# Kernel tuning notes

Measured on AMD Instinct MI355X. Metric: run time of the kernel, lower is better.

The kernel has to match this reference:

```python
import jax, jax.numpy as jnp
import numpy as np

N_HEAD = 16
N_KV_HEAD = 4
N_EMBD = 2048
HEAD_DIM = N_EMBD // N_HEAD  # 128
RMS_EPS = float(np.finfo(np.float32).eps)  # torch F.rms_norm default eps


def _apply_rotary(x, cos, sin):
    # x: [B,T,H,D]; cos/sin: [1,T,1,D/2]
    d = x.shape[-1] // 2
    x1, x2 = x[..., :d], x[..., d:]
    y1 = x1 * cos + x2 * sin
    y2 = -x1 * sin + x2 * cos
    return jnp.concatenate([y1, y2], axis=-1)


def _rms_norm(x):
    var = jnp.mean(jnp.square(x), axis=-1, keepdims=True)
    return x * jax.lax.rsqrt(var + RMS_EPS)


def setup_inputs() -> dict:
    key = jax.random.key(0)
    ks = jax.random.split(key, 7)
    B, T = 2, 2048
    x = jax.random.normal(ks[0], (B, T, N_EMBD), dtype=jnp.float32)
    cos = jax.random.normal(ks[1], (1, T, 1, HEAD_DIM // 2), dtype=jnp.float32)
    sin = jax.random.normal(ks[2], (1, T, 1, HEAD_DIM // 2), dtype=jnp.float32)
    s = 1.0 / np.sqrt(N_EMBD)
    Wq = jax.random.normal(ks[3], (N_HEAD * HEAD_DIM, N_EMBD), dtype=jnp.float32) * s
    Wk = jax.random.normal(ks[4], (N_KV_HEAD * HEAD_DIM, N_EMBD), dtype=jnp.float32) * s
    Wv = jax.random.normal(ks[5], (N_KV_HEAD * HEAD_DIM, N_EMBD), dtype=jnp.float32) * s
    Wo = jax.random.normal(ks[6], (N_EMBD, N_EMBD), dtype=jnp.float32) * s
    return {"x": x, "cos": cos, "sin": sin, "Wq": Wq, "Wk": Wk, "Wv": Wv, "Wo": Wo}


def reference(x, cos, sin, Wq, Wk, Wv, Wo):
    B, T, C = x.shape
    q = (x @ Wq.T).reshape(B, T, N_HEAD, HEAD_DIM)
    k = (x @ Wk.T).reshape(B, T, N_KV_HEAD, HEAD_DIM)
    v = (x @ Wv.T).reshape(B, T, N_KV_HEAD, HEAD_DIM)
    q = _rms_norm(_apply_rotary(q, cos, sin))
    k = _rms_norm(_apply_rotary(k, cos, sin))
    # to [B,H,T,D]; expand kv heads for GQA
    q = q.transpose(0, 2, 1, 3)
    k = k.transpose(0, 2, 1, 3)
    v = v.transpose(0, 2, 1, 3)
    g = N_HEAD // N_KV_HEAD
    k = jnp.repeat(k, g, axis=1)
    v = jnp.repeat(v, g, axis=1)
    scale = 1.0 / np.sqrt(HEAD_DIM)
    scores = jnp.einsum("bhtd,bhsd->bhts", q, k) * scale
    causal = jnp.tril(jnp.ones((T, T), dtype=bool))
    scores = jnp.where(causal, scores, -jnp.inf)
    attn = jax.nn.softmax(scores, axis=-1)
    y = jnp.einsum("bhts,bhsd->bhtd", attn, v)
    y = y.transpose(0, 2, 1, 3).reshape(B, T, C)
    return y @ Wo.T
```

## Files before the change

kernel.cpp:

```cpp
#include <hip/hip_runtime.h>
#include <hip/hip_bf16.h>
#include <stdint.h>

#define B_   2
#define T_   2048
#define CEMB 2048
#define H_   16
#define HKV_ 4
#define D_   128

typedef __attribute__((ext_vector_type(8))) short bf16x8;
typedef __attribute__((ext_vector_type(4))) float f32x4;
typedef __attribute__((ext_vector_type(16))) float f32x16;

#if __has_builtin(__builtin_amdgcn_exp2f)
#define EXP2(x) __builtin_amdgcn_exp2f(x)
#else
#define EXP2(x) exp2f(x)
#endif

__device__ __forceinline__ unsigned short f2b(float f) {
  union { float f; unsigned u; } v; v.f = f;
  unsigned r = v.u + 0x7FFFu + ((v.u >> 16) & 1u);
  return (unsigned short)(r >> 16);
}
__device__ __forceinline__ float b2f(unsigned short u) {
  union { unsigned u; float f; } v; v.u = ((unsigned)u) << 16; return v.f;
}
__device__ __forceinline__ unsigned cvtpk(float lo, float hi) {
  unsigned r;
  asm("v_cvt_pk_bf16_f32 %0, %1, %2" : "=v"(r) : "v"(lo), "v"(hi));
  return r;
}

#if __has_builtin(__builtin_amdgcn_permlane32_swap)
__device__ __forceinline__ void pl32(unsigned& a, unsigned& b) {
  auto r = __builtin_amdgcn_permlane32_swap(a, b, false, false);
  a = r[0]; b = r[1];
}
#else
__device__ __forceinline__ void pl32(unsigned& a, unsigned& b) {
  const bool hih = (threadIdx.x & 32) != 0;
  unsigned sa = __shfl_xor(a, 32), sb = __shfl_xor(b, 32);
  unsigned na = hih ? sb : a;
  unsigned nb = hih ? b : sa;
  a = na; b = nb;
}
#endif

__device__ __forceinline__ void gl16(const void* g, void* l) {
  __builtin_amdgcn_global_load_lds(
      (const __attribute__((address_space(1))) unsigned int*)g,
      (__attribute__((address_space(3))) unsigned int*)l, 16, 0, 0);
}

#define FENCE() asm volatile("" ::: "memory")

__global__ void cvt_kernel(const float* __restrict__ src,
                           unsigned short* __restrict__ dst, int n4) {
  int i = blockIdx.x * blockDim.x + threadIdx.x;
  const int stride = gridDim.x * blockDim.x;
  for (; i < n4; i += stride) {
    float4 v = ((const float4*)src)[i];
    ushort4 o;
    o.x = f2b(v.x); o.y = f2b(v.y); o.z = f2b(v.z); o.w = f2b(v.w);
    ((ushort4*)dst)[i] = o;
  }
}

__global__ __launch_bounds__(512, 2)
void gemm256(const unsigned short* __restrict__ A,
             const unsigned short* __restrict__ W,
             void* __restrict__ Cmat, int M, int N, int K, int obf16) {
  __shared__ alignas(16) unsigned short As[2][2][128][64];
  __shared__ alignas(16) unsigned short Bs[2][2][128][64];

  const int tid  = threadIdx.x;
  const int lane = tid & 63;
  const int w    = tid >> 6;
  const int wr   = w >> 2;
  const int wc   = w & 3;
  const int l16  = lane & 15, g4 = lane >> 4;
  const int srow = lane >> 3;
  const int schk = lane & 7;

  const int gx  = gridDim.x;
  const int nwg = gx * gridDim.y;
  const int lin = blockIdx.y * gx + blockIdx.x;
  const int cpx = nwg >> 3;
  const int swz = (lin & 7) * cpx + (lin >> 3);
  const int m0 = (swz / gx) * 256;
  const int n0 = (swz % gx) * 256;

  const unsigned short* Ap = A + (size_t)m0 * K;
  const unsigned short* Wp = W + (size_t)n0 * K;
  const int nk = K >> 6;

  f32x4 acc[8][4] = {};

  auto stA = [&](int ts, int h) {
    const unsigned short* g = Ap + (size_t)(h * 128 + w * 8 + srow) * K
                                 + ts * 64 + ((schk ^ srow) << 3);
    unsigned short* l = &As[ts & 1][h][w * 8][0];
    gl16(g, l);
    gl16(g + (size_t)64 * K, l + 64 * 64);
  };
  auto stB = [&](int ts, int h) {
    const unsigned short* g = Wp + (size_t)(h * 128 + w * 8 + srow) * K
                                 + ts * 64 + ((schk ^ srow) << 3);
    unsigned short* l = &Bs[ts & 1][h][w * 8][0];
    gl16(g, l);
    gl16(g + (size_t)64 * K, l + 64 * 64);
  };

  stA(0, 0); stB(0, 0); stA(0, 1); stB(0, 1);
  stA(1, 0); stB(1, 0);
  asm volatile("s_waitcnt vmcnt(4)" ::: "memory");
  __builtin_amdgcn_s_barrier();
  FENCE();

  for (int tau = 0; tau < nk; ++tau) {
    const int buf = tau & 1;
    bf16x8 af[4][2], bf0[2][2], bf1[2][2];
    #pragma unroll
    for (int mi = 0; mi < 4; ++mi) {
      const int har = (mi * 2 + wr) * 16 + l16;
      #pragma unroll
      for (int ks = 0; ks < 2; ++ks)
        af[mi][ks] = *(const bf16x8*)&As[buf][0][har][((ks * 4 + g4) ^ (l16 & 7)) << 3];
    }
    #pragma unroll
    for (int ni = 0; ni < 2; ++ni) {
      const int hbr = (ni * 4 + wc) * 16 + l16;
      #pragma unroll
      for (int ks = 0; ks < 2; ++ks)
        bf0[ni][ks] = *(const bf16x8*)&Bs[buf][0][hbr][((ks * 4 + g4) ^ (l16 & 7)) << 3];
    }
    if (tau + 1 < nk) stA(tau + 1, 1);
    __builtin_amdgcn_s_barrier();
    asm volatile("s_waitcnt lgkmcnt(0)" ::: "memory");
    __builtin_amdgcn_s_setprio(1);
    #pragma unroll
    for (int mi = 0; mi < 4; ++mi) {
      #pragma unroll
      for (int ni = 0; ni < 2; ++ni) {
        f32x4 t = acc[mi][ni];
        t = __builtin_amdgcn_mfma_f32_16x16x32_bf16(af[mi][0], bf0[ni][0], t, 0, 0, 0);
        t = __builtin_amdgcn_mfma_f32_16x16x32_bf16(af[mi][1], bf0[ni][1], t, 0, 0, 0);
        acc[mi][ni] = t;
      }
    }
    __builtin_amdgcn_s_setprio(0);
    __builtin_amdgcn_s_barrier();
    FENCE();
    #pragma unroll
    for (int ni = 0; ni < 2; ++ni) {
      const int hbr = (ni * 4 + wc) * 16 + l16;
      #pragma unroll
      for (int ks = 0; ks < 2; ++ks)
        bf1[ni][ks] = *(const bf16x8*)&Bs[buf][1][hbr][((ks * 4 + g4) ^ (l16 & 7)) << 3];
    }
    if (tau + 1 < nk) stB(tau + 1, 1);
    __builtin_amdgcn_s_barrier();
    asm volatile("s_waitcnt lgkmcnt(0)" ::: "memory");
    __builtin_amdgcn_s_setprio(1);
    #pragma unroll
    for (int mi = 0; mi < 4; ++mi) {
      #pragma unroll
      for (int ni = 0; ni < 2; ++ni) {
        f32x4 t = acc[mi][2 + ni];
        t = __builtin_amdgcn_mfma_f32_16x16x32_bf16(af[mi][0], bf1[ni][0], t, 0, 0, 0);
        t = __builtin_amdgcn_mfma_f32_16x16x32_bf16(af[mi][1], bf1[ni][1], t, 0, 0, 0);
        acc[mi][2 + ni] = t;
      }
    }
    __builtin_amdgcn_s_setprio(0);
    __builtin_amdgcn_s_barrier();
    FENCE();
    #pragma unroll
    for (int mi = 0; mi < 4; ++mi) {
      const int har = (mi * 2 + wr) * 16 + l16;
      #pragma unroll
      for (int ks = 0; ks < 2; ++ks)
        af[mi][ks] = *(const bf16x8*)&As[buf][1][har][((ks * 4 + g4) ^ (l16 & 7)) << 3];
    }
    if (tau + 2 < nk) stA(tau + 2, 0);
    __builtin_amdgcn_s_barrier();
    asm volatile("s_waitcnt lgkmcnt(0)" ::: "memory");
    __builtin_amdgcn_s_setprio(1);
    #pragma unroll
    for (int mi = 0; mi < 4; ++mi) {
      #pragma unroll
      for (int ni = 0; ni < 2; ++ni) {
        f32x4 t = acc[4 + mi][2 + ni];
        t = __builtin_amdgcn_mfma_f32_16x16x32_bf16(af[mi][0], bf1[ni][0], t, 0, 0, 0);
        t = __builtin_amdgcn_mfma_f32_16x16x32_bf16(af[mi][1], bf1[ni][1], t, 0, 0, 0);
        acc[4 + mi][2 + ni] = t;
      }
    }
    __builtin_amdgcn_s_setprio(0);
    __builtin_amdgcn_s_barrier();
    FENCE();
    if (tau + 2 < nk) stB(tau + 2, 0);
    __builtin_amdgcn_s_barrier();
    __builtin_amdgcn_s_setprio(1);
    #pragma unroll
    for (int mi = 0; mi < 4; ++mi) {
      #pragma unroll
      for (int ni = 0; ni < 2; ++ni) {
        f32x4 t = acc[4 + mi][ni];
        t = __builtin_amdgcn_mfma_f32_16x16x32_bf16(af[mi][0], bf0[ni][0], t, 0, 0, 0);
        t = __builtin_amdgcn_mfma_f32_16x16x32_bf16(af[mi][1], bf0[ni][1], t, 0, 0, 0);
        acc[4 + mi][ni] = t;
      }
    }
    __builtin_amdgcn_s_setprio(0);
    if (tau + 2 < nk) asm volatile("s_waitcnt vmcnt(4)" ::: "memory");
    else              asm volatile("s_waitcnt vmcnt(0)" ::: "memory");
    __builtin_amdgcn_s_barrier();
    FENCE();
  }

  #pragma unroll
  for (int fr = 0; fr < 8; ++fr) {
    #pragma unroll
    for (int fc = 0; fc < 4; ++fc) {
      const int row = m0 + (fr * 2 + wr) * 16 + g4 * 4;
      const int col = n0 + (fc * 4 + wc) * 16 + l16;
      if (obf16) {
        unsigned short* Cb = (unsigned short*)Cmat;
        #pragma unroll
        for (int r = 0; r < 4; ++r)
          Cb[(size_t)(row + r) * N + col] = f2b(acc[fr][fc][r]);
      } else {
        float* Cf = (float*)Cmat;
        #pragma unroll
        for (int r = 0; r < 4; ++r)
          Cf[(size_t)(row + r) * N + col] = acc[fr][fc][r];
      }
    }
  }
}

__global__ __launch_bounds__(128)
void rope_norm(const unsigned short* __restrict__ X, int rstride,
               const float* __restrict__ Cos, const float* __restrict__ Sin,
               unsigned short* __restrict__ Out, int Hn, float out_scale) {
  const int idx = blockIdx.x;
  const int h  = idx % Hn;
  const int bt = idx / Hn;
  const int t  = bt & (T_ - 1);
  const int b  = bt >> 11;
  const int d  = threadIdx.x;
  const unsigned short* src = X + (size_t)bt * rstride + h * D_;
  float y;
  if (d < 64) {
    float x1 = b2f(src[d]), x2 = b2f(src[d + 64]);
    float c = Cos[t * 64 + d], s = Sin[t * 64 + d];
    y = x1 * c + x2 * s;
  } else {
    int dd = d - 64;
    float x1 = b2f(src[dd]), x2 = b2f(src[d]);
    float c = Cos[t * 64 + dd], s = Sin[t * 64 + dd];
    y = -x1 * s + x2 * c;
  }
  float ss = y * y;
  #pragma unroll
  for (int m = 32; m; m >>= 1) ss += __shfl_xor(ss, m);
  __shared__ float red[2];
  if ((d & 63) == 0) red[d >> 6] = ss;
  __syncthreads();
  const float tot  = red[0] + red[1];
  const float rinv = rsqrtf(tot * (1.0f / 128.0f) + 1.1920929e-7f) * out_scale;
  Out[(((size_t)b * Hn + h) * T_ + t) * D_ + d] = f2b(y * rinv);
}

__global__ __launch_bounds__(256)
void vtrans(const unsigned short* __restrict__ Vf, int rstride,
            unsigned short* __restrict__ Vt) {
  __shared__ float tile[32][65];
  const int t0 = blockIdx.x * 64;
  const int d0 = blockIdx.y * 32;
  const int bh = blockIdx.z;
  const int b = bh >> 2, hk = bh & 3;
  const int tid = threadIdx.x;
  {
    const int di = tid & 31, ts = tid >> 5;
    #pragma unroll
    for (int i = 0; i < 8; ++i) {
      int tt = ts + i * 8;
      tile[di][tt] = b2f(Vf[(size_t)(b * T_ + t0 + tt) * rstride + hk * D_ + d0 + di]);
    }
  }
  __syncthreads();
  {
    const int ti = tid & 63, ds = tid >> 6;
    #pragma unroll
    for (int i = 0; i < 8; ++i) {
      int dd = ds * 8 + i;
      Vt[((size_t)bh * D_ + d0 + dd) * T_ + t0 + ti] = f2b(tile[dd][ti]);
    }
  }
}

#define KVB 128

__global__ __launch_bounds__(512)
void attn_kernel(const unsigned short* __restrict__ Qn,
                 const unsigned short* __restrict__ Kn,
                 const unsigned short* __restrict__ Vt,
                 unsigned short* __restrict__ Yb) {
  __shared__ alignas(16) unsigned short Ks[2][KVB][D_];
  __shared__ alignas(16) unsigned short Vs[2][D_][KVB];

  const int tid = threadIdx.x;
  const int lane = tid & 63;
  const int w = tid >> 6;
  const int wq  = w & 3;
  const int kvg = w >> 2;
  const int l31 = lane & 31;
  const int hi  = lane >> 5;
  const int bh = blockIdx.x;
  const int by = blockIdx.y;
  const int qt = (by < 8) ? by : 23 - by;
  const int b = bh >> 4, h = bh & 15;
  const int hk = h >> 2;

  const unsigned short* kp = Kn + ((size_t)(b * HKV_ + hk) * T_) * D_;
  const unsigned short* vp = Vt + ((size_t)(b * HKV_ + hk) * D_) * T_;

  const int r4 = lane >> 4, c16 = lane & 15;

  const int t0 = qt * 128;
  const int qrow0 = t0 + wq * 32;
  const int qmax = qrow0 + 31;
  const int nt = qt + 1;
  const int qglob = qrow0 + l31;

  const unsigned short* qp = Qn + ((size_t)bh * T_ + qrow0) * D_;
  bf16x8 qf[8];
  #pragma unroll
  for (int ds = 0; ds < 8; ++ds)
    qf[ds] = *(const bf16x8*)(qp + (size_t)l31 * D_ + ds * 16 + hi * 8);

  f32x16 o[4] = {};
  float l_lane = 0.f;

  auto stage = [&](int tt) {
    const int buf = tt & 1;
    const int kv = tt * KVB;
    #pragma unroll
    for (int j = 0; j < 4; ++j) {
      const int row = w * 16 + j * 4 + r4;
      const int cg = c16 ^ (row & 7);
      gl16(kp + (size_t)(kv + row) * D_ + cg * 8, &Ks[buf][w * 16 + j * 4][0]);
    }
    #pragma unroll
    for (int j = 0; j < 4; ++j) {
      const int row = w * 16 + j * 4 + r4;
      const int cg = c16 ^ (row & 7);
      gl16(vp + (size_t)row * T_ + kv + cg * 8, &Vs[buf][w * 16 + j * 4][0]);
    }
  };

  stage(0);

  union PAu { unsigned u[4]; bf16x8 v; };

  for (int t = 0; t < nt; ++t) {
    __syncthreads();
    if (t + 1 < nt) stage(t + 1);
    const int kbase = t * KVB + kvg * 64;
    if (kbase <= qmax) {
      const unsigned short (*kb)[D_]  = Ks[t & 1];
      const unsigned short (*vbp)[KVB] = Vs[t & 1];
      f32x16 s0 = {}, s1 = {};
      #pragma unroll
      for (int ds = 0; ds < 8; ++ds) {
        const int key0 = kvg * 64 + l31;
        const int key1 = kvg * 64 + 32 + l31;
        bf16x8 k0 = *(const bf16x8*)&kb[key0][(((ds * 2 + hi) ^ (key0 & 7)) << 3)];
        bf16x8 k1 = *(const bf16x8*)&kb[key1][(((ds * 2 + hi) ^ (key1 & 7)) << 3)];
        s0 = __builtin_amdgcn_mfma_f32_32x32x16_bf16(k0, qf[ds], s0, 0, 0, 0);
        s1 = __builtin_amdgcn_mfma_f32_32x32x16_bf16(k1, qf[ds], s1, 0, 0, 0);
      }
      const bool need_mask = (kbase + 63 > qrow0);
      float e0[16], e1[16];
      float ls = 0.f;
      #pragma unroll
      for (int r = 0; r < 16; ++r) {
        const int crow = (r & 3) + 8 * (r >> 2) + 4 * hi;
        float v0 = EXP2(s0[r]);
        float v1 = EXP2(s1[r]);
        if (need_mask) {
          v0 = (kbase + crow      <= qglob) ? v0 : 0.f;
          v1 = (kbase + 32 + crow <= qglob) ? v1 : 0.f;
        }
        e0[r] = v0; e1[r] = v1;
        ls += v0 + v1;
      }
      l_lane += ls;
      PAu pa[4];
      {
        unsigned a0 = cvtpk(e0[0],  e0[1]),  a1 = cvtpk(e0[2],  e0[3]);
        unsigned b0 = cvtpk(e0[4],  e0[5]),  b1 = cvtpk(e0[6],  e0[7]);
        unsigned c0 = cvtpk(e0[8],  e0[9]),  c1 = cvtpk(e0[10], e0[11]);
        unsigned d0 = cvtpk(e0[12], e0[13]), d1 = cvtpk(e0[14], e0[15]);
        pl32(a0, b0); pl32(a1, b1); pl32(c0, d0); pl32(c1, d1);
        pa[0].u[0] = a0; pa[0].u[1] = a1; pa[0].u[2] = b0; pa[0].u[3] = b1;
        pa[1].u[0] = c0; pa[1].u[1] = c1; pa[1].u[2] = d0; pa[1].u[3] = d1;
      }
      {
        unsigned a0 = cvtpk(e1[0],  e1[1]),  a1 = cvtpk(e1[2],  e1[3]);
        unsigned b0 = cvtpk(e1[4],  e1[5]),  b1 = cvtpk(e1[6],  e1[7]);
        unsigned c0 = cvtpk(e1[8],  e1[9]),  c1 = cvtpk(e1[10], e1[11]);
        unsigned d0 = cvtpk(e1[12], e1[13]), d1 = cvtpk(e1[14], e1[15]);
        pl32(a0, b0); pl32(a1, b1); pl32(c0, d0); pl32(c1, d1);
        pa[2].u[0] = a0; pa[2].u[1] = a1; pa[2].u[2] = b0; pa[2].u[3] = b1;
        pa[3].u[0] = c0; pa[3].u[1] = c1; pa[3].u[2] = d0; pa[3].u[3] = d1;
      }
      #pragma unroll
      for (int ks = 0; ks < 4; ++ks) {
        #pragma unroll
        for (int db = 0; db < 4; ++db) {
          const int d = db * 32 + l31;
          const int c = (kvg * 8 + ks * 2 + hi) ^ (d & 7);
          bf16x8 vf = *(const bf16x8*)&vbp[d][c << 3];
          o[db] = __builtin_amdgcn_mfma_f32_32x32x16_bf16(pa[ks].v, vf, o[db], 0, 0, 0);
        }
      }
    }
  }

  const float lfull = l_lane + __shfl_xor(l_lane, 32);
  __syncthreads();
  float* obuf = (float*)&Ks[0][0][0];
  float* lbuf = (float*)&Vs[0][0][0];
  if (w >= 4) {
    const int base = (w - 4) * 4096;
    #pragma unroll
    for (int r = 0; r < 16; ++r)
      #pragma unroll
      for (int db = 0; db < 4; ++db)
        obuf[base + (r * 4 + db) * 64 + lane] = o[db][r];
    if (hi == 0) lbuf[(w - 4) * 32 + l31] = lfull;
  }
  __syncthreads();
  if (w < 4) {
    const int base = w * 4096;
    const float ltot = lfull + lbuf[w * 32 + l31];
    const float invq = 1.0f / ltot;
    #pragma unroll
    for (int r = 0; r < 16; ++r) {
      const int crow = (r & 3) + 8 * (r >> 2) + 4 * hi;
      const float inv = __shfl(invq, crow);
      unsigned short* yrow = Yb + ((size_t)(b * T_ + qrow0 + crow) * CEMB) + h * D_;
      #pragma unroll
      for (int db = 0; db < 4; ++db)
        yrow[db * 32 + l31] = f2b((o[db][r] + obuf[base + (r * 4 + db) * 64 + lane]) * inv);
    }
  }
}

extern "C" void kernel_launch(void* const* d_in, const int* in_sizes, int n_in,
                              void* d_out, int out_size, void* d_ws, size_t ws_size,
                              hipStream_t stream) {
  const float* x    = (const float*)d_in[0];
  const float* cosp = (const float*)d_in[1];
  const float* sinp = (const float*)d_in[2];
  const float* Wq   = (const float*)d_in[3];
  const float* Wk   = (const float*)d_in[4];
  const float* Wv   = (const float*)d_in[5];
  const float* Wo   = (const float*)d_in[6];
  float* out = (float*)d_out;

  char* ws = (char*)d_ws;
  size_t off = 0;
  auto alloc = [&](size_t bytes) {
    void* p = ws + off;
    off += (bytes + 255) & ~(size_t)255;
    return p;
  };
  const size_t MT = (size_t)B_ * T_;
  const int NQKV = 3072;
  unsigned short* xb    = (unsigned short*)alloc(MT * CEMB * 2);
  unsigned short* wqkvb = (unsigned short*)alloc((size_t)NQKV * 2048 * 2);
  unsigned short* wob   = (unsigned short*)alloc((size_t)2048 * 2048 * 2);
  unsigned short* qkvb  = (unsigned short*)alloc(MT * NQKV * 2);
  unsigned short* qn    = (unsigned short*)alloc((size_t)B_ * H_ * T_ * D_ * 2);
  unsigned short* kn    = (unsigned short*)alloc((size_t)B_ * HKV_ * T_ * D_ * 2);
  unsigned short* vt    = (unsigned short*)alloc((size_t)B_ * HKV_ * D_ * T_ * 2);
  unsigned short* yb    = (unsigned short*)alloc(MT * CEMB * 2);

  cvt_kernel<<<2048, 256, 0, stream>>>(x,  xb, (int)(MT * CEMB / 4));
  cvt_kernel<<<1024, 256, 0, stream>>>(Wq, wqkvb,                2048 * 2048 / 4);
  cvt_kernel<<<256,  256, 0, stream>>>(Wk, wqkvb + 2048 * 2048,  512 * 2048 / 4);
  cvt_kernel<<<256,  256, 0, stream>>>(Wv, wqkvb + 2560 * 2048,  512 * 2048 / 4);
  cvt_kernel<<<1024, 256, 0, stream>>>(Wo, wob,                  2048 * 2048 / 4);

  gemm256<<<dim3(NQKV / 256, 4096 / 256), 512, 0, stream>>>(xb, wqkvb, qkvb, 4096, NQKV, 2048, 1);

  rope_norm<<<4096 * H_,   128, 0, stream>>>(qkvb,        NQKV, cosp, sinp, qn, H_,   0.1275174324f);
  rope_norm<<<4096 * HKV_, 128, 0, stream>>>(qkvb + 2048, NQKV, cosp, sinp, kn, HKV_, 1.0f);
  vtrans<<<dim3(T_ / 64, D_ / 32, B_ * HKV_), 256, 0, stream>>>(qkvb + 2560, NQKV, vt);

  attn_kernel<<<dim3(B_ * H_, 16), 512, 0, stream>>>(qn, kn, vt, yb);

  gemm256<<<dim3(2048 / 256, 4096 / 256), 512, 0, stream>>>(yb, wob, out, 4096, 2048, 2048, 0);
}
```

Before: 226.3 us.

## Restructure GEMM main loop into two-phase register double-buffered pipeline

Replaces the four-quadrant-per-k-tile GEMM loop, which had four barrier phases, with two phases per k-tile. A and B fragments for the next tile are held in ping-pong register buffers (X/Y), and the loop is unrolled by two to swap them. Each phase issues the global-to-LDS prefetch two tiles ahead and runs 32 MFMAs (4x4 blocks). This halves barrier count and increases MFMA work between syncs, but raises VGPR pressure with more fragment registers. It also waits vmcnt(0) each phase, which may expose global load latency. The loop assumes nk is even.

```diff
diff --git a/kernel.cpp b/kernel.cpp
--- a/kernel.cpp
+++ b/kernel.cpp
@@ -113,112 +113,108 @@
     gl16(g + (size_t)64 * K, l + 64 * 64);
   };
 
+  bf16x8 afAX[4][2], afAY[4][2], bfX[4][2], bfY[4][2];
+
   stA(0, 0); stB(0, 0); stA(0, 1); stB(0, 1);
-  stA(1, 0); stB(1, 0);
-  asm volatile("s_waitcnt vmcnt(4)" ::: "memory");
+  stA(1, 0); stB(1, 0); stA(1, 1); stB(1, 1);
+  asm volatile("s_waitcnt vmcnt(0)" ::: "memory");
   __builtin_amdgcn_s_barrier();
   FENCE();
-
-  for (int tau = 0; tau < nk; ++tau) {
-    const int buf = tau & 1;
-    bf16x8 af[4][2], bf0[2][2], bf1[2][2];
+  #pragma unroll
+  for (int mi = 0; mi < 4; ++mi) {
+    const int har = (mi * 2 + wr) * 16 + l16;
+    #pragma unroll
+    for (int ks = 0; ks < 2; ++ks)
+      afAX[mi][ks] = *(const bf16x8*)&As[0][0][har][((ks * 4 + g4) ^ (l16 & 7)) << 3];
+  }
+  #pragma unroll
+  for (int ni = 0; ni < 4; ++ni) {
+    const int hb = ni >> 1;
+    const int hbr = ((ni & 1) * 4 + wc) * 16 + l16;
+    #pragma unroll
+    for (int ks = 0; ks < 2; ++ks)
+      bfX[ni][ks] = *(const bf16x8*)&Bs[0][hb][hbr][((ks * 4 + g4) ^ (l16 & 7)) << 3];
+  }
+  asm volatile("s_waitcnt lgkmcnt(0)" ::: "memory");
+  __builtin_amdgcn_s_barrier();
+  FENCE();
+
+  auto ktile = [&](bf16x8 (*afA)[2], bf16x8 (*afA2)[2],
+                   bf16x8 (*bfc)[2], bf16x8 (*bfn)[2], int tau, int buf) {
+    bf16x8 afB[4][2];
+    if (tau + 1 < nk) {
+      #pragma unroll
+      for (int ni = 0; ni < 2; ++ni) {
+        const int hbr = (ni * 4 + wc) * 16 + l16;
+        #pragma unroll
+        for (int ks = 0; ks < 2; ++ks)
+          bfn[ni][ks] = *(const bf16x8*)&Bs[buf ^ 1][0][hbr][((ks * 4 + g4) ^ (l16 & 7)) << 3];
+      }
+    }
     #pragma unroll
     for (int mi = 0; mi < 4; ++mi) {
       const int har = (mi * 2 + wr) * 16 + l16;
       #pragma unroll
       for (int ks = 0; ks < 2; ++ks)
-        af[mi][ks] = *(const bf16x8*)&As[buf][0][har][((ks * 4 + g4) ^ (l16 & 7)) << 3];
-    }
-    #pragma unroll
-    for (int ni = 0; ni < 2; ++ni) {
-      const int hbr = (ni * 4 + wc) * 16 + l16;
-      #pragma unroll
-      for (int ks = 0; ks < 2; ++ks)
-        bf0[ni][ks] = *(const bf16x8*)&Bs[buf][0][hbr][((ks * 4 + g4) ^ (l16 & 7)) << 3];
-    }
-    if (tau + 1 < nk) stA(tau + 1, 1);
-    __builtin_amdgcn_s_barrier();
+        afB[mi][ks] = *(const bf16x8*)&As[buf][1][har][((ks * 4 + g4) ^ (l16 & 7)) << 3];
+    }
+    if (tau + 2 < nk) { stA(tau + 2, 0); stB(tau + 2, 0); }
+    __builtin_amdgcn_s_setprio(1);
+    #pragma unroll
+    for (int mi = 0; mi < 4; ++mi) {
+      #pragma unroll
+      for (int ni = 0; ni < 4; ++ni) {
+        f32x4 t = acc[mi][ni];
+        t = __builtin_amdgcn_mfma_f32_16x16x32_bf16(afA[mi][0], bfc[ni][0], t, 0, 0, 0);
+        t = __builtin_amdgcn_mfma_f32_16x16x32_bf16(afA[mi][1], bfc[ni][1], t, 0, 0, 0);
+        acc[mi][ni] = t;
+      }
+    }
+    __builtin_amdgcn_s_setprio(0);
     asm volatile("s_waitcnt lgkmcnt(0)" ::: "memory");
-    __builtin_amdgcn_s_setprio(1);
-    #pragma unroll
-    for (int mi = 0; mi < 4; ++mi) {
-      #pragma unroll
-      for (int ni = 0; ni < 2; ++ni) {
-        f32x4 t = acc[mi][ni];
-        t = __builtin_amdgcn_mfma_f32_16x16x32_bf16(af[mi][0], bf0[ni][0], t, 0, 0, 0);
-        t = __builtin_amdgcn_mfma_f32_16x16x32_bf16(af[mi][1], bf0[ni][1], t, 0, 0, 0);
-        acc[mi][ni] = t;
-      }
-    }
-    __builtin_amdgcn_s_setprio(0);
+    asm volatile("s_waitcnt vmcnt(0)" ::: "memory");
+    __builtin_amdgcn_sched_barrier(0);
     __builtin_amdgcn_s_barrier();
     FENCE();
-    #pragma unroll
-    for (int ni = 0; ni < 2; ++ni) {
-      const int hbr = (ni * 4 + wc) * 16 + l16;
-      #pragma unroll
-      for (int ks = 0; ks < 2; ++ks)
-        bf1[ni][ks] = *(const bf16x8*)&Bs[buf][1][hbr][((ks * 4 + g4) ^ (l16 & 7)) << 3];
-    }
-    if (tau + 1 < nk) stB(tau + 1, 1);
-    __builtin_amdgcn_s_barrier();
+    if (tau + 1 < nk) {
+      #pragma unroll
+      for (int mi = 0; mi < 4; ++mi) {
+        const int har = (mi * 2 + wr) * 16 + l16;
+        #pragma unroll
+        for (int ks = 0; ks < 2; ++ks)
+          afA2[mi][ks] = *(const bf16x8*)&As[buf ^ 1][0][har][((ks * 4 + g4) ^ (l16 & 7)) << 3];
+      }
+      #pragma unroll
+      for (int ni = 0; ni < 2; ++ni) {
+        const int hbr = (ni * 4 + wc) * 16 + l16;
+        #pragma unroll
+        for (int ks = 0; ks < 2; ++ks)
+          bfn[2 + ni][ks] = *(const bf16x8*)&Bs[buf ^ 1][1][hbr][((ks * 4 + g4) ^ (l16 & 7)) << 3];
+      }
+    }
+    if (tau + 2 < nk) { stA(tau + 2, 1); stB(tau + 2, 1); }
+    __builtin_amdgcn_s_setprio(1);
+    #pragma unroll
+    for (int mi = 0; mi < 4; ++mi) {
+      #pragma unroll
+      for (int ni = 0; ni < 4; ++ni) {
+        f32x4 t = acc[4 + mi][ni];
+        t = __builtin_amdgcn_mfma_f32_16x16x32_bf16(afB[mi][0], bfc[ni][0], t, 0, 0, 0);
+        t = __builtin_amdgcn_mfma_f32_16x16x32_bf16(afB[mi][1], bfc[ni][1], t, 0, 0, 0);
+        acc[4 + mi][ni] = t;
+      }
+    }
+    __builtin_amdgcn_s_setprio(0);
     asm volatile("s_waitcnt lgkmcnt(0)" ::: "memory");
-    __builtin_amdgcn_s_setprio(1);
-    #pragma unroll
-    for (int mi = 0; mi < 4; ++mi) {
-      #pragma unroll
-      for (int ni = 0; ni < 2; ++ni) {
-        f32x4 t = acc[mi][2 + ni];
-        t = __builtin_amdgcn_mfma_f32_16x16x32_bf16(af[mi][0], bf1[ni][0], t, 0, 0, 0);
-        t = __builtin_amdgcn_mfma_f32_16x16x32_bf16(af[mi][1], bf1[ni][1], t, 0, 0, 0);
-        acc[mi][2 + ni] = t;
-      }
-    }
-    __builtin_amdgcn_s_setprio(0);
+    asm volatile("s_waitcnt vmcnt(0)" ::: "memory");
+    __builtin_amdgcn_sched_barrier(0);
     __builtin_amdgcn_s_barrier();
     FENCE();
-    #pragma unroll
-    for (int mi = 0; mi < 4; ++mi) {
-      const int har = (mi * 2 + wr) * 16 + l16;
-      #pragma unroll
-      for (int ks = 0; ks < 2; ++ks)
-        af[mi][ks] = *(const bf16x8*)&As[buf][1][har][((ks * 4 + g4) ^ (l16 & 7)) << 3];
-    }
-    if (tau + 2 < nk) stA(tau + 2, 0);
-    __builtin_amdgcn_s_barrier();
-    asm volatile("s_waitcnt lgkmcnt(0)" ::: "memory");
-    __builtin_amdgcn_s_setprio(1);
-    #pragma unroll
-    for (int mi = 0; mi < 4; ++mi) {
-      #pragma unroll
-      for (int ni = 0; ni < 2; ++ni) {
-        f32x4 t = acc[4 + mi][2 + ni];
-        t = __builtin_amdgcn_mfma_f32_16x16x32_bf16(af[mi][0], bf1[ni][0], t, 0, 0, 0);
-        t = __builtin_amdgcn_mfma_f32_16x16x32_bf16(af[mi][1], bf1[ni][1], t, 0, 0, 0);
-        acc[4 + mi][2 + ni] = t;
-      }
-    }
-    __builtin_amdgcn_s_setprio(0);
-    __builtin_amdgcn_s_barrier();
-    FENCE();
-    if (tau + 2 < nk) stB(tau + 2, 0);
-    __builtin_amdgcn_s_barrier();
-    __builtin_amdgcn_s_setprio(1);
-    #pragma unroll
-    for (int mi = 0; mi < 4; ++mi) {
-      #pragma unroll
-      for (int ni = 0; ni < 2; ++ni) {
-        f32x4 t = acc[4 + mi][ni];
-        t = __builtin_amdgcn_mfma_f32_16x16x32_bf16(af[mi][0], bf0[ni][0], t, 0, 0, 0);
-        t = __builtin_amdgcn_mfma_f32_16x16x32_bf16(af[mi][1], bf0[ni][1], t, 0, 0, 0);
-        acc[4 + mi][ni] = t;
-      }
-    }
-    __builtin_amdgcn_s_setprio(0);
-    if (tau + 2 < nk) asm volatile("s_waitcnt vmcnt(4)" ::: "memory");
-    else              asm volatile("s_waitcnt vmcnt(0)" ::: "memory");
-    __builtin_amdgcn_s_barrier();
-    FENCE();
+  };
+
+  for (int tau = 0; tau < nk; tau += 2) {
+    ktile(afAX, afAY, bfX, bfY, tau,     0);
+    ktile(afAY, afAX, bfY, bfX, tau + 1, 1);
   }
 
   #pragma unroll
```

New measurement: 614.3 us. 171% more time.
